# Optimization experiments

Hardware: AMD Instinct MI355X
Metric: run time of the kernel (lower is better)

## Reference

```python
import jax, jax.numpy as jnp
import numpy as np

N_NODES = 50000
N_EDGES = 800000
F = 64
EPS = 1e-5


def batchnorm(x, gamma, beta):
    # training-mode BatchNorm1d: batch mean, biased variance
    mu = jnp.mean(x, axis=0)
    var = jnp.mean((x - mu) ** 2, axis=0)
    return gamma * (x - mu) * jax.lax.rsqrt(var + EPS) + beta


def setup_inputs() -> dict:
    key = jax.random.key(0)
    ks = jax.random.split(key, 10)
    s = 1.0 / np.sqrt(3 * F)
    return {
        "node_feats": jax.random.normal(ks[0], (N_NODES, F), jnp.float32),
        "edge_feats": jax.random.normal(ks[1], (N_EDGES, F), jnp.float32),
        "src": jax.random.randint(ks[2], (N_EDGES,), 0, N_NODES, jnp.int32),
        "dst": jax.random.randint(ks[3], (N_EDGES,), 0, N_NODES, jnp.int32),
        "W_mlpt": jax.random.uniform(ks[4], (3 * F, F), jnp.float32, -s, s),
        "b_mlpt": jnp.zeros((F,), jnp.float32),
        "g_mlpt": jnp.ones((F,), jnp.float32),
        "be_mlpt": jnp.zeros((F,), jnp.float32),
        "W_gate": jax.random.uniform(ks[5], (3 * F, F), jnp.float32, -s, s),
        "b_gate": jnp.zeros((F,), jnp.float32),
        "g_gate": jnp.ones((F,), jnp.float32),
        "be_gate": jnp.zeros((F,), jnp.float32),
        "g_node": jnp.ones((F,), jnp.float32),
        "be_node": jnp.zeros((F,), jnp.float32),
    }


def reference(node_feats, edge_feats, src, dst,
              W_mlpt, b_mlpt, g_mlpt, be_mlpt,
              W_gate, b_gate, g_gate, be_gate,
              g_node, be_node):
    # edge-wise gather + concat: [E, 3F]
    h_cat = jnp.concatenate(
        [node_feats[src], node_feats[dst], edge_feats], axis=1)
    # two small MLPs: Linear + BN + activation (dropout p=0)
    h_mlpt = jax.nn.sigmoid(batchnorm(h_cat @ W_mlpt + b_mlpt, g_mlpt, be_mlpt))
    h_gate = jax.nn.softplus(batchnorm(h_cat @ W_gate + b_gate, g_gate, be_gate))
    h_upd = h_mlpt * h_gate  # [E, F]
    # scatter-sum messages onto destination nodes
    agg = jax.ops.segment_sum(h_upd, dst, num_segments=N_NODES)  # [N, F]
    node_out = jax.nn.sigmoid(batchnorm(agg, g_node, be_node) + node_feats)
    return (node_out, edge_feats)
```

## Files before the change

### kernel.cpp

```cpp
#include <hip/hip_runtime.h>

#define E_TOT   800000
#define NN      50000
#define FF      64

typedef __attribute__((ext_vector_type(8))) short  short8;
typedef __attribute__((ext_vector_type(4))) float  f32x4;

__device__ __forceinline__ unsigned short f2bf(float f) {
  union { float f; unsigned int u; } v; v.f = f;
  unsigned int r = v.u + 0x7fffu + ((v.u >> 16) & 1u);
  return (unsigned short)(r >> 16);
}

__device__ __forceinline__ unsigned int pkbf(float a, float b) {
  unsigned int r;
  asm("v_cvt_pk_bf16_f32 %0, %1, %2" : "=v"(r) : "v"(a), "v"(b));
  return r;
}

__device__ __forceinline__ void atomic_pk_bf16(unsigned short* p, unsigned int v) {
  asm volatile("global_atomic_pk_add_bf16 %0, %1, off" :: "v"(p), "v"(v) : "memory");
}

__device__ __forceinline__ float bflo(unsigned int u) { return __uint_as_float(u << 16); }
__device__ __forceinline__ float bfhi(unsigned int u) { return __uint_as_float(u & 0xffff0000u); }

__device__ __forceinline__ float sigmoidf_(float x) {
  return 1.f / (1.f + __expf(-x));
}

__global__ void pack_w(const float* __restrict__ Wm, const float* __restrict__ Wg,
                       unsigned short* __restrict__ Wp) {
  int t = blockIdx.x * 256 + threadIdx.x;
  if (t >= 3072) return;
  int lane = t & 63;
  int kk   = (t >> 6) % 6;
  int mnt  = t / 384;
  const float* W = (mnt >> 2) ? Wg : Wm;
  int nt  = mnt & 3;
  int col = nt * 16 + (lane & 15);
  int kb  = kk * 32 + (lane >> 4) * 8;
  #pragma unroll
  for (int j = 0; j < 8; ++j)
    Wp[t * 8 + j] = f2bf(W[(kb + j) * 64 + col]);
}

__global__ __launch_bounds__(256, 5)
void edge_gemm(const float* __restrict__ nodef, const float* __restrict__ edgef,
               const int* __restrict__ src, const int* __restrict__ dst,
               const unsigned short* __restrict__ Wp,
               float* __restrict__ stats,
               uint4* __restrict__ Yw,
               float* __restrict__ outE, int write_copy)
{
  __shared__ unsigned short sh[64 * 200];
  __shared__ float red[4 * 256];

  const int tid = threadIdx.x;
  const int e0  = blockIdx.x * 64;
  const int row = tid >> 2;
  const int cq  = tid & 3;

  const int s = src[e0 + row], d = dst[e0 + row];
  const float* ps = nodef + (size_t)s * 64 + cq * 4;
  const float* pd = nodef + (size_t)d * 64 + cq * 4;
  const float* pe = edgef + (size_t)(e0 + row) * 64 + cq * 4;
  unsigned short* sp = &sh[row * 200 + cq * 4];

  float4 ev[4];
  #pragma unroll
  for (int it = 0; it < 4; ++it) {
    float4 v0 = *(const float4*)(ps + it * 16);
    float4 v1 = *(const float4*)(pd + it * 16);
    float4 v2 = *(const float4*)(pe + it * 16);
    ev[it] = v2;
    *(uint2*)(sp +   0 + it * 16) = make_uint2(pkbf(v0.x, v0.y), pkbf(v0.z, v0.w));
    *(uint2*)(sp +  64 + it * 16) = make_uint2(pkbf(v1.x, v1.y), pkbf(v1.z, v1.w));
    *(uint2*)(sp + 128 + it * 16) = make_uint2(pkbf(v2.x, v2.y), pkbf(v2.z, v2.w));
  }
  if (write_copy) {
    float4* op = (float4*)(outE + (size_t)e0 * 64 + (size_t)row * 64 + cq * 4);
    #pragma unroll
    for (int it = 0; it < 4; ++it) op[it * 4] = ev[it];
  }

  asm volatile("s_waitcnt lgkmcnt(0)" ::: "memory");

  const int w = tid >> 6, lane = tid & 63;
  f32x4 acc[8] = {};
  const unsigned short* abase = &sh[(w * 16 + (lane & 15)) * 200 + (lane >> 4) * 8];
  const short8* wp = (const short8*)Wp;

  #pragma unroll
  for (int kk = 0; kk < 6; ++kk) {
    short8 a = *(const short8*)(abase + kk * 32);
    #pragma unroll
    for (int nt = 0; nt < 8; ++nt) {
      short8 b = wp[(nt * 6 + kk) * 64 + lane];
      acc[nt] = __builtin_amdgcn_mfma_f32_16x16x32_bf16(a, b, acc[nt], 0, 0, 0);
    }
  }

  uint4* yb = Yw + (((size_t)blockIdx.x * 4 + w) * 4) * 64 + lane;
  #pragma unroll
  for (int ntp = 0; ntp < 4; ++ntp) {
    uint4 q;
    q.x = pkbf(acc[2 * ntp][0],     acc[2 * ntp][1]);
    q.y = pkbf(acc[2 * ntp][2],     acc[2 * ntp][3]);
    q.z = pkbf(acc[2 * ntp + 1][0], acc[2 * ntp + 1][1]);
    q.w = pkbf(acc[2 * ntp + 1][2], acc[2 * ntp + 1][3]);
    yb[ntp * 64] = q;
  }

  #pragma unroll
  for (int nt = 0; nt < 8; ++nt) {
    float sv = acc[nt][0] + acc[nt][1] + acc[nt][2] + acc[nt][3];
    float qv = acc[nt][0] * acc[nt][0] + acc[nt][1] * acc[nt][1] +
               acc[nt][2] * acc[nt][2] + acc[nt][3] * acc[nt][3];
    sv += __shfl_xor(sv, 16); sv += __shfl_xor(sv, 32);
    qv += __shfl_xor(qv, 16); qv += __shfl_xor(qv, 32);
    if ((lane >> 4) == 0) {
      red[w * 256 + nt * 16 + lane]       = sv;
      red[w * 256 + 128 + nt * 16 + lane] = qv;
    }
  }
  __syncthreads();
  float v = red[tid] + red[256 + tid] + red[512 + tid] + red[768 + tid];
  atomicAdd(&stats[(blockIdx.x & 63) * 256 + tid], v);
}

__global__ void finalize_edge(const float* __restrict__ stats,
                              const float* __restrict__ g_m, const float* __restrict__ be_m,
                              const float* __restrict__ g_g, const float* __restrict__ be_g,
                              float* __restrict__ coef) {
  int c = threadIdx.x;
  float s = 0.f, q = 0.f;
  for (int sl = 0; sl < 64; ++sl) { s += stats[sl * 256 + c]; q += stats[sl * 256 + 128 + c]; }
  float mu  = s * (1.f / E_TOT);
  float var = fmaxf(q * (1.f / E_TOT) - mu * mu, 0.f);
  float g   = (c < 64) ? g_m[c]  : g_g[c - 64];
  float be  = (c < 64) ? be_m[c] : be_g[c - 64];
  float a   = g * rsqrtf(var + 1e-5f);
  coef[c]       = a;
  coef[128 + c] = be - mu * a;
}

__global__ __launch_bounds__(256)
void edge_apply(const uint4* __restrict__ Yw, const int* __restrict__ dst,
                const float* __restrict__ coef,
                unsigned short* __restrict__ aggb)
{
  const int tid = threadIdx.x;
  const int w = tid >> 6, lane = tid & 63;
  const int e0 = blockIdx.x * 64;
  const int r0 = w * 16 + ((lane >> 4) << 2);
  const int4 dn = *(const int4*)&dst[e0 + r0];
  const int colb = lane & 15;
  const int par  = colb & 1;

  const uint4* yb = Yw + (((size_t)blockIdx.x * 4 + w) * 4) * 64 + lane;
  uint4 qm0 = yb[0], qm1 = yb[64], qg0 = yb[128], qg1 = yb[192];
  const unsigned int um[8] = {qm0.x, qm0.y, qm0.z, qm0.w, qm1.x, qm1.y, qm1.z, qm1.w};
  const unsigned int ug[8] = {qg0.x, qg0.y, qg0.z, qg0.w, qg1.x, qg1.y, qg1.z, qg1.w};
  const int dr[4] = {dn.x, dn.y, dn.z, dn.w};

  #pragma unroll
  for (int ntm = 0; ntm < 4; ++ntm) {
    const int col = ntm * 16 + colb;
    const float am = coef[col],      cm = coef[128 + col];
    const float ag = coef[64 + col], cg = coef[192 + col];
    float hv[4];
    #pragma unroll
    for (int p = 0; p < 2; ++p) {
      unsigned int m = um[ntm * 2 + p], g = ug[ntm * 2 + p];
      #pragma unroll
      for (int h = 0; h < 2; ++h) {
        float mv = h ? bfhi(m) : bflo(m);
        float gv = h ? bfhi(g) : bflo(g);
        float ym = fmaf(mv, am, cm);
        float yg = fmaf(gv, ag, cg);
        float sig = sigmoidf_(ym);
        float sp  = (yg > 20.f) ? yg : __logf(1.f + __expf(yg));
        hv[2 * p + h] = sig * sp;
      }
    }
    float pv[4];
    #pragma unroll
    for (int rr = 0; rr < 4; ++rr) pv[rr] = __shfl_xor(hv[rr], 1);
    const int colp = ntm * 16 + (colb & ~1);
    #pragma unroll
    for (int rr = 0; rr < 2; ++rr) {
      int rx = par * 2 + rr;
      float lo = par ? pv[rx] : hv[rx];
      float hi = par ? hv[rx] : pv[rx];
      atomic_pk_bf16(&aggb[(size_t)dr[rx] * 64 + colp], pkbf(lo, hi));
    }
  }
}

__global__ void node_stats(const unsigned int* __restrict__ aggu, float* __restrict__ nstats) {
  __shared__ float rs0[256], rq0[256], rs1[256], rq1[256];
  int tid = threadIdx.x;
  int cp = tid & 31;
  float s0 = 0.f, q0 = 0.f, s1 = 0.f, q1 = 0.f;
  for (int r = blockIdx.x * 8 + (tid >> 5); r < NN; r += gridDim.x * 8) {
    unsigned int u = aggu[r * 32 + cp];
    float v0 = bflo(u), v1 = bfhi(u);
    s0 += v0; q0 += v0 * v0; s1 += v1; q1 += v1 * v1;
  }
  rs0[tid] = s0; rq0[tid] = q0; rs1[tid] = s1; rq1[tid] = q1;
  __syncthreads();
  if (tid < 32) {
    s0 = 0.f; q0 = 0.f; s1 = 0.f; q1 = 0.f;
    #pragma unroll
    for (int k = 0; k < 8; ++k) {
      s0 += rs0[tid + 32 * k]; q0 += rq0[tid + 32 * k];
      s1 += rs1[tid + 32 * k]; q1 += rq1[tid + 32 * k];
    }
    int slot = blockIdx.x & 31;
    atomicAdd(&nstats[slot * 128 + 2 * tid],      s0);
    atomicAdd(&nstats[slot * 128 + 2 * tid + 1],  s1);
    atomicAdd(&nstats[slot * 128 + 64 + 2 * tid],     q0);
    atomicAdd(&nstats[slot * 128 + 64 + 2 * tid + 1], q1);
  }
}

__global__ void finalize_node(const float* __restrict__ nstats,
                              const float* __restrict__ g_n, const float* __restrict__ be_n,
                              float* __restrict__ coefn) {
  int c = threadIdx.x;
  float s = 0.f, q = 0.f;
  for (int sl = 0; sl < 32; ++sl) { s += nstats[sl * 128 + c]; q += nstats[sl * 128 + 64 + c]; }
  float mu  = s * (1.f / NN);
  float var = fmaxf(q * (1.f / NN) - mu * mu, 0.f);
  float a   = g_n[c] * rsqrtf(var + 1e-5f);
  coefn[c]      = a;
  coefn[64 + c] = be_n[c] - mu * a;
}

__global__ void node_out_k(float* __restrict__ out, const unsigned int* __restrict__ aggu,
                           const float* __restrict__ nodef, const float* __restrict__ coefn) {
  int i  = blockIdx.x * 256 + threadIdx.x;
  int cb = (i & 15) * 4;
  uint2  u  = ((const uint2*)aggu)[i];
  float4 nf = ((const float4*)nodef)[i];
  float4 r;
  r.x = sigmoidf_(coefn[cb + 0] * bflo(u.x) + coefn[64 + cb + 0] + nf.x);
  r.y = sigmoidf_(coefn[cb + 1] * bfhi(u.x) + coefn[64 + cb + 1] + nf.y);
  r.z = sigmoidf_(coefn[cb + 2] * bflo(u.y) + coefn[64 + cb + 2] + nf.z);
  r.w = sigmoidf_(coefn[cb + 3] * bfhi(u.y) + coefn[64 + cb + 3] + nf.w);
  ((float4*)out)[i] = r;
}

extern "C" void kernel_launch(void* const* d_in, const int* in_sizes, int n_in,
                              void* d_out, int out_size, void* d_ws, size_t ws_size,
                              hipStream_t stream) {
  const float* nodef = (const float*)d_in[0];
  const float* edgef = (const float*)d_in[1];
  const int*   src   = (const int*)d_in[2];
  const int*   dst   = (const int*)d_in[3];
  const float* W_m   = (const float*)d_in[4];
  const float* g_m   = (const float*)d_in[6];
  const float* be_m  = (const float*)d_in[7];
  const float* W_g   = (const float*)d_in[8];
  const float* g_g   = (const float*)d_in[10];
  const float* be_g  = (const float*)d_in[11];
  const float* g_n   = (const float*)d_in[12];
  const float* be_n  = (const float*)d_in[13];

  float* out  = (float*)d_out;
  float* outE = out + (size_t)NN * FF;

  char* ws = (char*)d_ws;
  unsigned short* aggb = (unsigned short*)ws;
  float* stats  = (float*)(ws + 0x640000);
  float* coef   = (float*)(ws + 0x650000);
  float* nstats = (float*)(ws + 0x651000);
  float* coefn  = (float*)(ws + 0x655000);
  unsigned short* Wp = (unsigned short*)(ws + 0x656000);

  const size_t y_bytes = (size_t)E_TOT * 128 * 2;
  const int y_in_ws = (ws_size >= (size_t)0x700000 + y_bytes);
  uint4* Yw = y_in_ws ? (uint4*)(ws + 0x700000) : (uint4*)outE;

  hipMemsetAsync(aggb, 0, (size_t)NN * FF * 2, stream);
  hipMemsetAsync(stats, 0, 0x15200, stream);

  pack_w<<<12, 256, 0, stream>>>(W_m, W_g, Wp);
  edge_gemm<<<E_TOT / 64, 256, 0, stream>>>(nodef, edgef, src, dst, Wp,
                                            stats, Yw, outE, y_in_ws);
  finalize_edge<<<1, 128, 0, stream>>>(stats, g_m, be_m, g_g, be_g, coef);
  edge_apply<<<E_TOT / 64, 256, 0, stream>>>(Yw, dst, coef, aggb);
  if (!y_in_ws) {
    hipMemcpyAsync(outE, edgef, (size_t)E_TOT * FF * sizeof(float),
                   hipMemcpyDeviceToDevice, stream);
  }
  node_stats<<<512, 256, 0, stream>>>((const unsigned int*)aggb, nstats);
  finalize_node<<<1, 64, 0, stream>>>(nstats, g_n, be_n, coefn);
  node_out_k<<<NN * FF / 4 / 256, 256, 0, stream>>>(out, (const unsigned int*)aggb,
                                                    nodef, coefn);
}
```

Measured before the change: 419.4 us.

## Load MFMA A-operands directly from global memory, removing the LDS staging

Each lane now gathers its own MFMA A-fragment (8 contiguous floats per K-chunk for the src, dst and edge rows) straight from global memory and converts it to bf16 in registers. This drops the shared-memory tile and its write/read round trip, which also frees LDS so the launch-bounds occupancy hint is raised from 5 to 6. The per-lane global access pattern changes from fully row-coalesced float4s to strided 32-byte pieces, which may reduce coalescing efficiency. Register pressure also rises because all twelve float4 loads are held at once.

```diff
diff --git a/kernel.cpp b/kernel.cpp
--- a/kernel.cpp
+++ b/kernel.cpp
@@ -28,6 +28,12 @@
 
 __device__ __forceinline__ float sigmoidf_(float x) {
   return 1.f / (1.f + __expf(-x));
+}
+
+__device__ __forceinline__ short8 cvt8(float4 f0, float4 f1) {
+  uint4 u = make_uint4(pkbf(f0.x, f0.y), pkbf(f0.z, f0.w),
+                       pkbf(f1.x, f1.y), pkbf(f1.z, f1.w));
+  return __builtin_bit_cast(short8, u);
 }
 
 __global__ void pack_w(const float* __restrict__ Wm, const float* __restrict__ Wg,
@@ -46,7 +52,7 @@
     Wp[t * 8 + j] = f2bf(W[(kb + j) * 64 + col]);
 }
 
-__global__ __launch_bounds__(256, 5)
+__global__ __launch_bounds__(256, 6)
 void edge_gemm(const float* __restrict__ nodef, const float* __restrict__ edgef,
                const int* __restrict__ src, const int* __restrict__ dst,
                const unsigned short* __restrict__ Wp,
@@ -54,52 +60,43 @@
                uint4* __restrict__ Yw,
                float* __restrict__ outE, int write_copy)
 {
-  __shared__ unsigned short sh[64 * 200];
   __shared__ float red[4 * 256];
 
-  const int tid = threadIdx.x;
-  const int e0  = blockIdx.x * 64;
-  const int row = tid >> 2;
-  const int cq  = tid & 3;
-
-  const int s = src[e0 + row], d = dst[e0 + row];
-  const float* ps = nodef + (size_t)s * 64 + cq * 4;
-  const float* pd = nodef + (size_t)d * 64 + cq * 4;
-  const float* pe = edgef + (size_t)(e0 + row) * 64 + cq * 4;
-  unsigned short* sp = &sh[row * 200 + cq * 4];
-
-  float4 ev[4];
-  #pragma unroll
-  for (int it = 0; it < 4; ++it) {
-    float4 v0 = *(const float4*)(ps + it * 16);
-    float4 v1 = *(const float4*)(pd + it * 16);
-    float4 v2 = *(const float4*)(pe + it * 16);
-    ev[it] = v2;
-    *(uint2*)(sp +   0 + it * 16) = make_uint2(pkbf(v0.x, v0.y), pkbf(v0.z, v0.w));
-    *(uint2*)(sp +  64 + it * 16) = make_uint2(pkbf(v1.x, v1.y), pkbf(v1.z, v1.w));
-    *(uint2*)(sp + 128 + it * 16) = make_uint2(pkbf(v2.x, v2.y), pkbf(v2.z, v2.w));
-  }
+  const int tid  = threadIdx.x;
+  const int w    = tid >> 6, lane = tid & 63;
+  const int g    = lane >> 4, r = lane & 15;
+  const int e    = blockIdx.x * 64 + w * 16 + r;
+
+  const int s = src[e], d = dst[e];
+
+  const float4* qs = (const float4*)(nodef + (size_t)s * 64 + g * 8);
+  const float4* qd = (const float4*)(nodef + (size_t)d * 64 + g * 8);
+  const float4* qe = (const float4*)(edgef + (size_t)e * 64 + g * 8);
+
+  float4 s0 = qs[0], s1 = qs[1], s2 = qs[8], s3 = qs[9];
+  float4 d0 = qd[0], d1 = qd[1], d2 = qd[8], d3 = qd[9];
+  float4 e0f = qe[0], e1f = qe[1], e2f = qe[8], e3f = qe[9];
+
   if (write_copy) {
-    float4* op = (float4*)(outE + (size_t)e0 * 64 + (size_t)row * 64 + cq * 4);
-    #pragma unroll
-    for (int it = 0; it < 4; ++it) op[it * 4] = ev[it];
-  }
-
-  asm volatile("s_waitcnt lgkmcnt(0)" ::: "memory");
-
-  const int w = tid >> 6, lane = tid & 63;
+    float4* op = (float4*)(outE + (size_t)e * 64 + g * 8);
+    op[0] = e0f; op[1] = e1f; op[8] = e2f; op[9] = e3f;
+  }
+
+  const short8 aS0 = cvt8(s0, s1),   aS1 = cvt8(s2, s3);
+  const short8 aD0 = cvt8(d0, d1),   aD1 = cvt8(d2, d3);
+  const short8 aE0 = cvt8(e0f, e1f), aE1 = cvt8(e2f, e3f);
+
+  const short8* wp = (const short8*)Wp;
   f32x4 acc[8] = {};
-  const unsigned short* abase = &sh[(w * 16 + (lane & 15)) * 200 + (lane >> 4) * 8];
-  const short8* wp = (const short8*)Wp;
-
-  #pragma unroll
-  for (int kk = 0; kk < 6; ++kk) {
-    short8 a = *(const short8*)(abase + kk * 32);
-    #pragma unroll
-    for (int nt = 0; nt < 8; ++nt) {
-      short8 b = wp[(nt * 6 + kk) * 64 + lane];
-      acc[nt] = __builtin_amdgcn_mfma_f32_16x16x32_bf16(a, b, acc[nt], 0, 0, 0);
-    }
+
+  #pragma unroll
+  for (int nt = 0; nt < 8; ++nt) {
+    acc[nt] = __builtin_amdgcn_mfma_f32_16x16x32_bf16(aS0, wp[(nt * 6 + 0) * 64 + lane], acc[nt], 0, 0, 0);
+    acc[nt] = __builtin_amdgcn_mfma_f32_16x16x32_bf16(aS1, wp[(nt * 6 + 1) * 64 + lane], acc[nt], 0, 0, 0);
+    acc[nt] = __builtin_amdgcn_mfma_f32_16x16x32_bf16(aD0, wp[(nt * 6 + 2) * 64 + lane], acc[nt], 0, 0, 0);
+    acc[nt] = __builtin_amdgcn_mfma_f32_16x16x32_bf16(aD1, wp[(nt * 6 + 3) * 64 + lane], acc[nt], 0, 0, 0);
+    acc[nt] = __builtin_amdgcn_mfma_f32_16x16x32_bf16(aE0, wp[(nt * 6 + 4) * 64 + lane], acc[nt], 0, 0, 0);
+    acc[nt] = __builtin_amdgcn_mfma_f32_16x16x32_bf16(aE1, wp[(nt * 6 + 5) * 64 + lane], acc[nt], 0, 0, 0);
   }
 
   uint4* yb = Yw + (((size_t)blockIdx.x * 4 + w) * 4) * 64 + lane;
```

After: 430.6 us. 2.7% more time.

## Privatize bf16 scatter accumulator into multiple workspace copies to cut atomic contention

Applied to the files above, without the earlier changes.

The edge_apply scatter now spreads its packed bf16 atomic adds across up to eight private copies of the node aggregate buffer, chosen by block index. The copy count depends on how much workspace is free. node_stats then sums the copies back into the primary buffer before computing batch-norm statistics. This targets atomic contention and serialization on shared destination rows, at the cost of extra memsets, extra reads during the reduction, and more memory footprint.

```diff
diff --git a/kernel.cpp b/kernel.cpp
--- a/kernel.cpp
+++ b/kernel.cpp
@@ -80,7 +80,7 @@
     *(uint2*)(sp + 128 + it * 16) = make_uint2(pkbf(v2.x, v2.y), pkbf(v2.z, v2.w));
   }
   if (write_copy) {
-    float4* op = (float4*)(outE + (size_t)e0 * 64 + (size_t)row * 64 + cq * 4);
+    float4* op = (float4*)(outE + (size_t)(e0 + row) * 64 + cq * 4);
     #pragma unroll
     for (int it = 0; it < 4; ++it) op[it * 4] = ev[it];
   }
@@ -149,7 +149,8 @@
 __global__ __launch_bounds__(256)
 void edge_apply(const uint4* __restrict__ Yw, const int* __restrict__ dst,
                 const float* __restrict__ coef,
-                unsigned short* __restrict__ aggb)
+                unsigned short* __restrict__ aggb,
+                unsigned short* __restrict__ agg_ext, int cpmask)
 {
   const int tid = threadIdx.x;
   const int w = tid >> 6, lane = tid & 63;
@@ -158,6 +159,9 @@
   const int4 dn = *(const int4*)&dst[e0 + r0];
   const int colb = lane & 15;
   const int par  = colb & 1;
+
+  const int cp = blockIdx.x & cpmask;
+  unsigned short* base = (cp == 0) ? aggb : (agg_ext + (size_t)(cp - 1) * (NN * 64));
 
   const uint4* yb = Yw + (((size_t)blockIdx.x * 4 + w) * 4) * 64 + lane;
   uint4 qm0 = yb[0], qm1 = yb[64], qg0 = yb[128], qg1 = yb[192];
@@ -194,20 +198,27 @@
       int rx = par * 2 + rr;
       float lo = par ? pv[rx] : hv[rx];
       float hi = par ? hv[rx] : pv[rx];
-      atomic_pk_bf16(&aggb[(size_t)dr[rx] * 64 + colp], pkbf(lo, hi));
-    }
-  }
-}
-
-__global__ void node_stats(const unsigned int* __restrict__ aggu, float* __restrict__ nstats) {
+      atomic_pk_bf16(&base[(size_t)dr[rx] * 64 + colp], pkbf(lo, hi));
+    }
+  }
+}
+
+__global__ void node_stats(unsigned int* __restrict__ agg0,
+                           const unsigned int* __restrict__ agg_ext,
+                           int ncp, float* __restrict__ nstats) {
   __shared__ float rs0[256], rq0[256], rs1[256], rq1[256];
   int tid = threadIdx.x;
   int cp = tid & 31;
   float s0 = 0.f, q0 = 0.f, s1 = 0.f, q1 = 0.f;
   for (int r = blockIdx.x * 8 + (tid >> 5); r < NN; r += gridDim.x * 8) {
-    unsigned int u = aggu[r * 32 + cp];
-    float v0 = bflo(u), v1 = bfhi(u);
-    s0 += v0; q0 += v0 * v0; s1 += v1; q1 += v1 * v1;
+    unsigned int u = agg0[r * 32 + cp];
+    float c0 = bflo(u), c1 = bfhi(u);
+    for (int k = 1; k < ncp; ++k) {
+      unsigned int uk = agg_ext[(size_t)(k - 1) * (NN * 32) + r * 32 + cp];
+      c0 += bflo(uk); c1 += bfhi(uk);
+    }
+    if (ncp > 1) agg0[r * 32 + cp] = pkbf(c0, c1);
+    s0 += c0; q0 += c0 * c0; s1 += c1; q1 += c1 * c1;
   }
   rs0[tid] = s0; rq0[tid] = q0; rs1[tid] = s1; rq1[tid] = q1;
   __syncthreads();
@@ -284,19 +295,28 @@
   const int y_in_ws = (ws_size >= (size_t)0x700000 + y_bytes);
   uint4* Yw = y_in_ws ? (uint4*)(ws + 0x700000) : (uint4*)outE;
 
+  const size_t ext_off = y_in_ws ? ((size_t)0x700000 + y_bytes) : (size_t)0x700000;
+  unsigned short* agg_ext = (unsigned short*)(ws + ext_off);
+  size_t avail = (ws_size > ext_off) ? (ws_size - ext_off) : 0;
+  int extra = (int)(avail / 0x640000);
+  int ncp = (extra >= 7) ? 8 : (extra >= 3) ? 4 : (extra >= 1) ? 2 : 1;
+
   hipMemsetAsync(aggb, 0, (size_t)NN * FF * 2, stream);
+  if (ncp > 1)
+    hipMemsetAsync(agg_ext, 0, (size_t)(ncp - 1) * NN * FF * 2, stream);
   hipMemsetAsync(stats, 0, 0x15200, stream);
 
   pack_w<<<12, 256, 0, stream>>>(W_m, W_g, Wp);
   edge_gemm<<<E_TOT / 64, 256, 0, stream>>>(nodef, edgef, src, dst, Wp,
                                             stats, Yw, outE, y_in_ws);
   finalize_edge<<<1, 128, 0, stream>>>(stats, g_m, be_m, g_g, be_g, coef);
-  edge_apply<<<E_TOT / 64, 256, 0, stream>>>(Yw, dst, coef, aggb);
+  edge_apply<<<E_TOT / 64, 256, 0, stream>>>(Yw, dst, coef, aggb, agg_ext, ncp - 1);
   if (!y_in_ws) {
     hipMemcpyAsync(outE, edgef, (size_t)E_TOT * FF * sizeof(float),
                    hipMemcpyDeviceToDevice, stream);
   }
-  node_stats<<<512, 256, 0, stream>>>((const unsigned int*)aggb, nstats);
+  node_stats<<<512, 256, 0, stream>>>((unsigned int*)aggb, (const unsigned int*)agg_ext,
+                                      ncp, nstats);
   finalize_node<<<1, 64, 0, stream>>>(nstats, g_n, be_n, coefn);
   node_out_k<<<NN * FF / 4 / 256, 256, 0, stream>>>(out, (const unsigned int*)aggb,
                                                     nodef, coefn);
```

Measured after the change: 476.0 us. 13.5% more time.
